# Performance work log

Hardware: AMD Instinct MI355X
Metric: run time of the kernel (lower is better)

The kernel has to match this reference:

```python
import jax, jax.numpy as jnp
import numpy as np

B, S, E, H = 2, 2048, 1024, 16
D = E // H  # head_dim = 64
NEG = -1e10


def setup_inputs() -> dict:
    key = jax.random.key(0)
    ks = jax.random.split(key, 12)
    sc = 1.0 / np.sqrt(E)
    return {
        "query": jax.random.normal(ks[0], (B, S, E), jnp.float32),
        "key_": jax.random.normal(ks[1], (B, S, E), jnp.float32),
        "value": jax.random.normal(ks[2], (B, S, E), jnp.float32),
        "mask": jax.random.randint(ks[3], (B, S), 0, 2, jnp.int32),
        "Wq": jax.random.normal(ks[4], (E, E), jnp.float32) * sc,
        "bq": jnp.zeros((E,), jnp.float32),
        "Wk": jax.random.normal(ks[5], (E, E), jnp.float32) * sc,
        "bk": jnp.zeros((E,), jnp.float32),
        "Wv": jax.random.normal(ks[6], (E, E), jnp.float32) * sc,
        "bv": jnp.zeros((E,), jnp.float32),
        "Wo": jax.random.normal(ks[7], (E, E), jnp.float32) * sc,
        "bo": jnp.zeros((E,), jnp.float32),
    }


def reference(query, key_, value, mask, Wq, bq, Wk, bk, Wv, bv, Wo, bo):
    # Linear projections (torch Linear: x @ W^T + b)
    Q = (query @ Wq.T + bq).reshape(B, S, H, D)
    K = (key_ @ Wk.T + bk).reshape(B, S, H, D)
    V = (value @ Wv.T + bv).reshape(B, S, H, D)
    # [B, H, Sq, Sk] scores
    scores = jnp.einsum("bqhd,bkhd->bhqk", Q, K) / jnp.sqrt(jnp.float32(D))
    # Original sets rows of masked query positions AND columns of masked key
    # positions to -1e10 (set, not add; overlapping assignment is same value).
    pad = (mask == 0)  # [B, S]
    bad = pad[:, :, None] | pad[:, None, :]  # [B, Sq, Sk]
    scores = scores + jnp.where(bad, NEG, 0.0)[:, None, :, :]
    weights = jax.nn.softmax(scores, axis=-1)
    out = jnp.einsum("bhqk,bkhd->bqhd", weights, V).reshape(B, S, E)
    return out @ Wo.T + bo
```

## Files before the change

kernel.cpp:

```cpp
#include <hip/hip_runtime.h>

typedef __attribute__((ext_vector_type(4)))  float          f32x4;
typedef __attribute__((ext_vector_type(16))) float          f32x16;
typedef __attribute__((ext_vector_type(8)))  short          s16x8;
typedef __attribute__((ext_vector_type(4)))  unsigned short u16x4;
typedef __attribute__((ext_vector_type(8)))  unsigned short u16x8;

#define MFMA_BF16(a, b, c) __builtin_amdgcn_mfma_f32_16x16x32_bf16((a), (b), (c), 0, 0, 0)
#define MFMA32(a, b, c)    __builtin_amdgcn_mfma_f32_32x32x16_bf16((a), (b), (c), 0, 0, 0)

static constexpr int Bb = 2, Ss = 2048, Ee = 1024, Hh = 16, Dd = 64;
static constexpr size_t M4 = 4u * 1024 * 1024;
static constexpr size_t M1 = 1024 * 1024;

__device__ __forceinline__ unsigned short f2b(float f) {
    unsigned u = __builtin_bit_cast(unsigned, f);
    u += 0x7fffu + ((u >> 16) & 1u);
    return (unsigned short)(u >> 16);
}

__device__ __forceinline__ void gld_lds16(const unsigned short* g, unsigned short* l) {
    __builtin_amdgcn_global_load_lds(
        (const __attribute__((address_space(1))) unsigned int*)g,
        (__attribute__((address_space(3))) unsigned int*)l, 16, 0, 0);
}

struct CvtArgs { const float* src[7]; unsigned short* dst; };

__global__ __launch_bounds__(256) void cvt_bf16(CvtArgs a)
{
    size_t i = ((size_t)blockIdx.x * 256 + threadIdx.x) * 8;
    int seg; size_t off;
    if (i < 3 * M4) { seg = (int)(i / M4);          off = i % M4; }
    else            { size_t j = i - 3 * M4;
                      seg = 3 + (int)(j / M1);      off = j % M1; }
    const float* s = a.src[seg] + off;
    f32x4 x0 = *(const f32x4*)s;
    f32x4 x1 = *(const f32x4*)(s + 4);
    u16x8 o = (u16x8){f2b(x0[0]), f2b(x0[1]), f2b(x0[2]), f2b(x0[3]),
                      f2b(x1[0]), f2b(x1[1]), f2b(x1[2]), f2b(x1[3])};
    *(u16x8*)(a.dst + i) = o;
}

template <int OUT_MODE>
__device__ __forceinline__ void gemm_bf16_body(const unsigned short* __restrict__ A,
                                               const unsigned short* __restrict__ W,
                                               const float* __restrict__ bias,
                                               void* __restrict__ Cv)
{
    __shared__ __align__(16) unsigned short Al[128 * 32];
    __shared__ __align__(16) unsigned short Bl[128 * 32];

    const int tid  = threadIdx.x;
    const int lane = tid & 63;
    const int wid  = tid >> 6;
    const int quad = lane >> 4;
    const int lr   = lane & 15;
    const int wr   = (wid >> 1) * 64;
    const int wc   = (wid & 1) * 64;
    const int m0   = blockIdx.y * 128;
    const int n0   = blockIdx.x * 128;

    const int srow = wid * 32 + (lane >> 2);
    const int sk8  = (lane & 3) * 8;
    const unsigned short* gA = A + (size_t)(m0 + srow) * 1024 + sk8;
    const unsigned short* gW = W + (size_t)(n0 + srow) * 1024 + sk8;
    unsigned short* lA = &Al[wid * 1024];
    unsigned short* lW = &Bl[wid * 1024];

    f32x4 acc[4][4];
#pragma unroll
    for (int i = 0; i < 4; i++)
#pragma unroll
        for (int j = 0; j < 4; j++) acc[i][j] = (f32x4){0.f, 0.f, 0.f, 0.f};

    for (int ks = 0; ks < 1024; ks += 32) {
        __syncthreads();
        gld_lds16(gA + ks,              lA);
        gld_lds16(gA + ks + 16 * 1024,  lA + 512);
        gld_lds16(gW + ks,              lW);
        gld_lds16(gW + ks + 16 * 1024,  lW + 512);
        __syncthreads();

        s16x8 af[4], bf[4];
#pragma unroll
        for (int t = 0; t < 4; t++) {
            af[t] = *(const s16x8*)&Al[(wr + t * 16 + lr) * 32 + quad * 8];
            bf[t] = *(const s16x8*)&Bl[(wc + t * 16 + lr) * 32 + quad * 8];
        }
#pragma unroll
        for (int mt = 0; mt < 4; mt++)
#pragma unroll
            for (int nt = 0; nt < 4; nt++)
                acc[mt][nt] = MFMA_BF16(af[mt], bf[nt], acc[mt][nt]);
    }

#pragma unroll
    for (int mt = 0; mt < 4; mt++)
#pragma unroll
        for (int nt = 0; nt < 4; nt++) {
            int   col  = n0 + wc + nt * 16 + lr;
            float bcol = bias[col];
            int   rbase = m0 + wr + mt * 16 + quad * 4;
            if (OUT_MODE == 2) {
                int bb = rbase >> 11, s = rbase & 2047;
                u16x4 pk;
#pragma unroll
                for (int r = 0; r < 4; r++) pk[r] = f2b(acc[mt][nt][r] + bcol);
                *(u16x4*)&((unsigned short*)Cv)[((size_t)(bb * 1024 + col)) * 2048 + s] = pk;
            } else {
#pragma unroll
                for (int r = 0; r < 4; r++) {
                    float v = acc[mt][nt][r] + bcol;
                    if (OUT_MODE == 3) v *= 0.125f;
                    if (OUT_MODE == 0)
                        ((float*)Cv)[(size_t)(rbase + r) * 1024 + col] = v;
                    else
                        ((unsigned short*)Cv)[(size_t)(rbase + r) * 1024 + col] = f2b(v);
                }
            }
        }
}

struct GArgs {
    const unsigned short* A[3];
    const unsigned short* W[3];
    const float* bias[3];
    unsigned short* C[3];
};

__global__ __launch_bounds__(256) void proj_gemm(GArgs ga)
{
    int z = blockIdx.z;
    if (z == 2)
        gemm_bf16_body<2>(ga.A[2], ga.W[2], ga.bias[2], ga.C[2]);
    else if (z == 1)
        gemm_bf16_body<1>(ga.A[1], ga.W[1], ga.bias[1], ga.C[1]);
    else
        gemm_bf16_body<3>(ga.A[0], ga.W[0], ga.bias[0], ga.C[0]);
}

__global__ __launch_bounds__(256) void out_gemm(const unsigned short* __restrict__ A,
                                                const unsigned short* __restrict__ W,
                                                const float* __restrict__ bias,
                                                float* __restrict__ C)
{
    gemm_bf16_body<0>(A, W, bias, C);
}

__global__ __launch_bounds__(256)
void flash_attn(const unsigned short* __restrict__ Q,
                const unsigned short* __restrict__ K,
                const unsigned short* __restrict__ Vt,
                const int* __restrict__ mask,
                unsigned short* __restrict__ O)
{
    constexpr int   ST  = 72;
    constexpr float EPS = 9.31322575e-10f;
    __shared__ __align__(16) unsigned short Kl[64 * ST];
    __shared__ __align__(16) unsigned short Vl[64 * ST];
    __shared__ __align__(16) unsigned short Pl[128 * ST];
    __shared__ __align__(16) float mkf[2048];
    __shared__ float lsq[128];

    const int b  = blockIdx.z;
    const int h  = blockIdx.y;
    const int q0 = blockIdx.x * 128;

    const int tid  = threadIdx.x;
    const int lane = tid & 63;
    const int wid  = tid >> 6;
    const int l31  = lane & 31;
    const int hl   = lane >> 5;

    for (int i = tid; i < 2048; i += 256) mkf[i] = mask[b * 2048 + i] ? 1.f : 0.f;

    const unsigned short* qg =
        Q + (size_t)(b * 2048 + q0 + wid * 32 + l31) * 1024 + h * 64 + hl * 8;
    s16x8 qf[4];
#pragma unroll
    for (int db = 0; db < 4; db++) qf[db] = *(const s16x8*)(qg + db * 16);

    __syncthreads();
    const float mq = mkf[q0 + wid * 32 + l31];

    const int lk = (tid >> 3) * ST + (tid & 7) * 8;
    const unsigned short* gK = K  + (size_t)(b * 2048 + (tid >> 3)) * 1024 + h * 64 + (tid & 7) * 8;
    const unsigned short* gV = Vt + (size_t)(b * 1024 + h * 64 + (tid >> 3)) * 2048 + (tid & 7) * 8;

    float  lsum  = 0.f;
    f32x16 accO0 = (f32x16){0.f,0.f,0.f,0.f,0.f,0.f,0.f,0.f,0.f,0.f,0.f,0.f,0.f,0.f,0.f,0.f};
    f32x16 accO1 = accO0;

    unsigned short* plw = &Pl[wid * 32 * ST];

    for (int kt = 0; kt < 2048; kt += 64) {
        __syncthreads();
        *(u16x8*)&Kl[lk]           = *(const u16x8*)(gK + (size_t)kt * 1024);
        *(u16x8*)&Kl[lk + 32 * ST] = *(const u16x8*)(gK + (size_t)(kt + 32) * 1024);
        *(u16x8*)&Vl[lk]           = *(const u16x8*)(gV + kt);
        *(u16x8*)&Vl[lk + 32 * ST] = *(const u16x8*)(gV + kt + (size_t)32 * 2048);
        __syncthreads();

#pragma unroll
        for (int kt2 = 0; kt2 < 2; kt2++) {
            f32x16 st = (f32x16){0.f,0.f,0.f,0.f,0.f,0.f,0.f,0.f,
                                 0.f,0.f,0.f,0.f,0.f,0.f,0.f,0.f};
#pragma unroll
            for (int db = 0; db < 4; db++) {
                s16x8 kf = *(const s16x8*)&Kl[(kt2 * 32 + l31) * ST + db * 16 + hl * 8];
                st = MFMA32(kf, qf[db], st);
            }
#pragma unroll
            for (int rq = 0; rq < 4; rq++) {
                int   kb = kt2 * 32 + 4 * hl + 8 * rq;
                f32x4 m4 = *(const f32x4*)&mkf[kt + kb];
                unsigned u[4];
#pragma unroll
                for (int r = 0; r < 4; r++) {
                    float e = __expf(st[rq * 4 + r]);
                    float p = e * (m4[r] * mq) + EPS;
                    lsum += p;
                    u[r] = __builtin_bit_cast(unsigned, p) + 0x8000u;
                }
                uint2 w;
                w.x = __builtin_amdgcn_perm(u[1], u[0], 0x07060302u);
                w.y = __builtin_amdgcn_perm(u[3], u[2], 0x07060302u);
                *(uint2*)&plw[l31 * ST + kb] = w;
            }
        }

#pragma unroll
        for (int kb = 0; kb < 4; kb++) {
            s16x8 pf  = *(const s16x8*)&plw[l31 * ST + kb * 16 + hl * 8];
            s16x8 vf0 = *(const s16x8*)&Vl[l31 * ST + kb * 16 + hl * 8];
            s16x8 vf1 = *(const s16x8*)&Vl[(32 + l31) * ST + kb * 16 + hl * 8];
            accO0 = MFMA32(pf, vf0, accO0);
            accO1 = MFMA32(pf, vf1, accO1);
        }
    }

    lsum += __shfl_xor(lsum, 32, 64);
    if (lane < 32) lsq[wid * 32 + l31] = lsum;

#pragma unroll
    for (int dc = 0; dc < 2; dc++)
#pragma unroll
        for (int rq = 0; rq < 4; rq++) {
            f32x4 ls4 = *(const f32x4*)&lsq[wid * 32 + 4 * hl + 8 * rq];
#pragma unroll
            for (int r = 0; r < 4; r++) {
                int   qrow = 4 * hl + 8 * rq + r;
                float acc  = (dc == 0) ? accO0[rq * 4 + r] : accO1[rq * 4 + r];
                float val  = acc * __builtin_amdgcn_rcpf(ls4[r]);
                O[(size_t)(b * 2048 + q0 + wid * 32 + qrow) * 1024 + h * 64 +
                  dc * 32 + l31] = f2b(val);
            }
        }
}

extern "C" void kernel_launch(void* const* d_in, const int* in_sizes, int n_in,
                              void* d_out, int out_size, void* d_ws, size_t ws_size,
                              hipStream_t stream)
{
    const float* query = (const float*)d_in[0];
    const float* key_  = (const float*)d_in[1];
    const float* value = (const float*)d_in[2];
    const int*   mask  = (const int*)d_in[3];
    const float* Wq    = (const float*)d_in[4];
    const float* bq    = (const float*)d_in[5];
    const float* Wk    = (const float*)d_in[6];
    const float* bk    = (const float*)d_in[7];
    const float* Wv    = (const float*)d_in[8];
    const float* bv    = (const float*)d_in[9];
    const float* Wo    = (const float*)d_in[10];
    const float* bo    = (const float*)d_in[11];
    float* out = (float*)d_out;

    unsigned short* cvt = (unsigned short*)d_ws;
    unsigned short* Aq  = cvt;
    unsigned short* Ak  = cvt + M4;
    unsigned short* Av  = cvt + 2 * M4;
    unsigned short* Wqb = cvt + 3 * M4;
    unsigned short* Wkb = Wqb + M1;
    unsigned short* Wvb = Wkb + M1;
    unsigned short* Wob = Wvb + M1;
    unsigned short* Qb  = Wob + M1;
    unsigned short* Kb  = Qb + M4;
    unsigned short* Vt  = Kb + M4;
    unsigned short* Ab  = Vt + M4;

    CvtArgs ca;
    ca.src[0] = query; ca.src[1] = key_; ca.src[2] = value;
    ca.src[3] = Wq; ca.src[4] = Wk; ca.src[5] = Wv; ca.src[6] = Wo;
    ca.dst = cvt;
    cvt_bf16<<<dim3(8192), 256, 0, stream>>>(ca);

    GArgs ga;
    ga.A[0] = Aq;  ga.A[1] = Ak;  ga.A[2] = Av;
    ga.W[0] = Wqb; ga.W[1] = Wkb; ga.W[2] = Wvb;
    ga.bias[0] = bq; ga.bias[1] = bk; ga.bias[2] = bv;
    ga.C[0] = Qb; ga.C[1] = Kb; ga.C[2] = Vt;
    proj_gemm<<<dim3(8, 32, 3), 256, 0, stream>>>(ga);

    flash_attn<<<dim3(Ss / 128, Hh, Bb), 256, 0, stream>>>(Qb, Kb, Vt, mask, Ab);
    out_gemm<<<dim3(8, 32, 1), 256, 0, stream>>>(Ab, Wob, bo, out);
}
```

Baseline: 272.8 us.

## Halve attention query tile, precompute float mask, widen GEMM K-step, use exp2

After: 272.6 us. Within noise of the previous version (-0.1%).

```diff
diff --git a/kernel.cpp b/kernel.cpp
--- a/kernel.cpp
+++ b/kernel.cpp
@@ -25,15 +25,24 @@
         (__attribute__((address_space(3))) unsigned int*)l, 16, 0, 0);
 }
 
-struct CvtArgs { const float* src[7]; unsigned short* dst; };
+struct CvtArgs { const float* src[7]; unsigned short* dst;
+                 const int* mask; float* maskf; };
 
 __global__ __launch_bounds__(256) void cvt_bf16(CvtArgs a)
 {
+    if (blockIdx.x == 8192) {
+#pragma unroll
+        for (int j = 0; j < 16; j++) {
+            int idx = threadIdx.x + j * 256;
+            a.maskf[idx] = a.mask[idx] ? 1.f : 0.f;
+        }
+        return;
+    }
     size_t i = ((size_t)blockIdx.x * 256 + threadIdx.x) * 8;
     int seg; size_t off;
-    if (i < 3 * M4) { seg = (int)(i / M4);          off = i % M4; }
+    if (i < 3 * M4) { seg = (int)(i / M4);     off = i % M4; }
     else            { size_t j = i - 3 * M4;
-                      seg = 3 + (int)(j / M1);      off = j % M1; }
+                      seg = 3 + (int)(j / M1); off = j % M1; }
     const float* s = a.src[seg] + off;
     f32x4 x0 = *(const f32x4*)s;
     f32x4 x1 = *(const f32x4*)(s + 4);
@@ -48,8 +57,8 @@
                                                const float* __restrict__ bias,
                                                void* __restrict__ Cv)
 {
-    __shared__ __align__(16) unsigned short Al[128 * 32];
-    __shared__ __align__(16) unsigned short Bl[128 * 32];
+    __shared__ __align__(16) unsigned short Al0[128 * 32], Al1[128 * 32];
+    __shared__ __align__(16) unsigned short Bl0[128 * 32], Bl1[128 * 32];
 
     const int tid  = threadIdx.x;
     const int lane = tid & 63;
@@ -65,8 +74,8 @@
     const int sk8  = (lane & 3) * 8;
     const unsigned short* gA = A + (size_t)(m0 + srow) * 1024 + sk8;
     const unsigned short* gW = W + (size_t)(n0 + srow) * 1024 + sk8;
-    unsigned short* lA = &Al[wid * 1024];
-    unsigned short* lW = &Bl[wid * 1024];
+    unsigned short* lA0 = &Al0[wid * 1024]; unsigned short* lA1 = &Al1[wid * 1024];
+    unsigned short* lW0 = &Bl0[wid * 1024]; unsigned short* lW1 = &Bl1[wid * 1024];
 
     f32x4 acc[4][4];
 #pragma unroll
@@ -74,25 +83,34 @@
 #pragma unroll
         for (int j = 0; j < 4; j++) acc[i][j] = (f32x4){0.f, 0.f, 0.f, 0.f};
 
-    for (int ks = 0; ks < 1024; ks += 32) {
-        __syncthreads();
-        gld_lds16(gA + ks,              lA);
-        gld_lds16(gA + ks + 16 * 1024,  lA + 512);
-        gld_lds16(gW + ks,              lW);
-        gld_lds16(gW + ks + 16 * 1024,  lW + 512);
-        __syncthreads();
-
-        s16x8 af[4], bf[4];
-#pragma unroll
-        for (int t = 0; t < 4; t++) {
-            af[t] = *(const s16x8*)&Al[(wr + t * 16 + lr) * 32 + quad * 8];
-            bf[t] = *(const s16x8*)&Bl[(wc + t * 16 + lr) * 32 + quad * 8];
-        }
-#pragma unroll
-        for (int mt = 0; mt < 4; mt++)
-#pragma unroll
-            for (int nt = 0; nt < 4; nt++)
-                acc[mt][nt] = MFMA_BF16(af[mt], bf[nt], acc[mt][nt]);
+    for (int ks = 0; ks < 1024; ks += 64) {
+        __syncthreads();
+        gld_lds16(gA + ks,                   lA0);
+        gld_lds16(gA + ks + 16 * 1024,       lA0 + 512);
+        gld_lds16(gA + ks + 32,              lA1);
+        gld_lds16(gA + ks + 32 + 16 * 1024,  lA1 + 512);
+        gld_lds16(gW + ks,                   lW0);
+        gld_lds16(gW + ks + 16 * 1024,       lW0 + 512);
+        gld_lds16(gW + ks + 32,              lW1);
+        gld_lds16(gW + ks + 32 + 16 * 1024,  lW1 + 512);
+        __syncthreads();
+
+#pragma unroll
+        for (int sub = 0; sub < 2; sub++) {
+            const unsigned short* Als = sub ? Al1 : Al0;
+            const unsigned short* Bls = sub ? Bl1 : Bl0;
+            s16x8 af[4], bf[4];
+#pragma unroll
+            for (int t = 0; t < 4; t++) {
+                af[t] = *(const s16x8*)&Als[(wr + t * 16 + lr) * 32 + quad * 8];
+                bf[t] = *(const s16x8*)&Bls[(wc + t * 16 + lr) * 32 + quad * 8];
+            }
+#pragma unroll
+            for (int mt = 0; mt < 4; mt++)
+#pragma unroll
+                for (int nt = 0; nt < 4; nt++)
+                    acc[mt][nt] = MFMA_BF16(af[mt], bf[nt], acc[mt][nt]);
+        }
     }
 
 #pragma unroll
@@ -112,7 +130,7 @@
 #pragma unroll
                 for (int r = 0; r < 4; r++) {
                     float v = acc[mt][nt][r] + bcol;
-                    if (OUT_MODE == 3) v *= 0.125f;
+                    if (OUT_MODE == 3) v *= 0.180336884f;
                     if (OUT_MODE == 0)
                         ((float*)Cv)[(size_t)(rbase + r) * 1024 + col] = v;
                     else
@@ -132,12 +150,9 @@
 __global__ __launch_bounds__(256) void proj_gemm(GArgs ga)
 {
     int z = blockIdx.z;
-    if (z == 2)
-        gemm_bf16_body<2>(ga.A[2], ga.W[2], ga.bias[2], ga.C[2]);
-    else if (z == 1)
-        gemm_bf16_body<1>(ga.A[1], ga.W[1], ga.bias[1], ga.C[1]);
-    else
-        gemm_bf16_body<3>(ga.A[0], ga.W[0], ga.bias[0], ga.C[0]);
+    if (z == 2)      gemm_bf16_body<2>(ga.A[2], ga.W[2], ga.bias[2], ga.C[2]);
+    else if (z == 1) gemm_bf16_body<1>(ga.A[1], ga.W[1], ga.bias[1], ga.C[1]);
+    else             gemm_bf16_body<3>(ga.A[0], ga.W[0], ga.bias[0], ga.C[0]);
 }
 
 __global__ __launch_bounds__(256) void out_gemm(const unsigned short* __restrict__ A,
@@ -152,47 +167,44 @@
 void flash_attn(const unsigned short* __restrict__ Q,
                 const unsigned short* __restrict__ K,
                 const unsigned short* __restrict__ Vt,
-                const int* __restrict__ mask,
+                const float* __restrict__ maskf,
                 unsigned short* __restrict__ O)
 {
-    constexpr int   ST  = 72;
+    constexpr int   ST  = 76;
     constexpr float EPS = 9.31322575e-10f;
     __shared__ __align__(16) unsigned short Kl[64 * ST];
     __shared__ __align__(16) unsigned short Vl[64 * ST];
-    __shared__ __align__(16) unsigned short Pl[128 * ST];
-    __shared__ __align__(16) float mkf[2048];
-    __shared__ float lsq[128];
+    __shared__ __align__(16) unsigned short Pl[64 * ST];
+    __shared__ float lsq[4][32];
 
     const int b  = blockIdx.z;
     const int h  = blockIdx.y;
-    const int q0 = blockIdx.x * 128;
+    const int q0 = blockIdx.x * 64;
 
     const int tid  = threadIdx.x;
     const int lane = tid & 63;
     const int wid  = tid >> 6;
     const int l31  = lane & 31;
     const int hl   = lane >> 5;
-
-    for (int i = tid; i < 2048; i += 256) mkf[i] = mask[b * 2048 + i] ? 1.f : 0.f;
+    const int qh   = wid & 1;
+    const int kh   = wid >> 1;
 
     const unsigned short* qg =
-        Q + (size_t)(b * 2048 + q0 + wid * 32 + l31) * 1024 + h * 64 + hl * 8;
+        Q + (size_t)(b * 2048 + q0 + qh * 32 + l31) * 1024 + h * 64 + hl * 8;
     s16x8 qf[4];
 #pragma unroll
     for (int db = 0; db < 4; db++) qf[db] = *(const s16x8*)(qg + db * 16);
 
-    __syncthreads();
-    const float mq = mkf[q0 + wid * 32 + l31];
+    const float  mq  = maskf[b * 2048 + q0 + qh * 32 + l31];
+    const float* mkp = maskf + b * 2048;
 
     const int lk = (tid >> 3) * ST + (tid & 7) * 8;
     const unsigned short* gK = K  + (size_t)(b * 2048 + (tid >> 3)) * 1024 + h * 64 + (tid & 7) * 8;
     const unsigned short* gV = Vt + (size_t)(b * 1024 + h * 64 + (tid >> 3)) * 2048 + (tid & 7) * 8;
 
-    float  lsum  = 0.f;
-    f32x16 accO0 = (f32x16){0.f,0.f,0.f,0.f,0.f,0.f,0.f,0.f,0.f,0.f,0.f,0.f,0.f,0.f,0.f,0.f};
-    f32x16 accO1 = accO0;
-
-    unsigned short* plw = &Pl[wid * 32 * ST];
+    float  lsum = 0.f;
+    f32x16 accO = (f32x16){0.f,0.f,0.f,0.f,0.f,0.f,0.f,0.f,
+                           0.f,0.f,0.f,0.f,0.f,0.f,0.f,0.f};
 
     for (int kt = 0; kt < 2048; kt += 64) {
         __syncthreads();
@@ -202,61 +214,56 @@
         *(u16x8*)&Vl[lk + 32 * ST] = *(const u16x8*)(gV + kt + (size_t)32 * 2048);
         __syncthreads();
 
-#pragma unroll
-        for (int kt2 = 0; kt2 < 2; kt2++) {
-            f32x16 st = (f32x16){0.f,0.f,0.f,0.f,0.f,0.f,0.f,0.f,
-                                 0.f,0.f,0.f,0.f,0.f,0.f,0.f,0.f};
-#pragma unroll
-            for (int db = 0; db < 4; db++) {
-                s16x8 kf = *(const s16x8*)&Kl[(kt2 * 32 + l31) * ST + db * 16 + hl * 8];
-                st = MFMA32(kf, qf[db], st);
+        f32x16 st = (f32x16){0.f,0.f,0.f,0.f,0.f,0.f,0.f,0.f,
+                             0.f,0.f,0.f,0.f,0.f,0.f,0.f,0.f};
+#pragma unroll
+        for (int db = 0; db < 4; db++) {
+            s16x8 kf = *(const s16x8*)&Kl[(kh * 32 + l31) * ST + db * 16 + hl * 8];
+            st = MFMA32(kf, qf[db], st);
+        }
+#pragma unroll
+        for (int rq = 0; rq < 4; rq++) {
+            int   kb = 4 * hl + 8 * rq;
+            f32x4 m4 = *(const f32x4*)&mkp[kt + kh * 32 + kb];
+            unsigned u[4];
+#pragma unroll
+            for (int r = 0; r < 4; r++) {
+                float e = __builtin_amdgcn_exp2f(st[rq * 4 + r]);
+                float p = e * (m4[r] * mq) + EPS;
+                lsum += p;
+                u[r] = __builtin_bit_cast(unsigned, p) + 0x8000u;
             }
-#pragma unroll
-            for (int rq = 0; rq < 4; rq++) {
-                int   kb = kt2 * 32 + 4 * hl + 8 * rq;
-                f32x4 m4 = *(const f32x4*)&mkf[kt + kb];
-                unsigned u[4];
-#pragma unroll
-                for (int r = 0; r < 4; r++) {
-                    float e = __expf(st[rq * 4 + r]);
-                    float p = e * (m4[r] * mq) + EPS;
-                    lsum += p;
-                    u[r] = __builtin_bit_cast(unsigned, p) + 0x8000u;
-                }
-                uint2 w;
-                w.x = __builtin_amdgcn_perm(u[1], u[0], 0x07060302u);
-                w.y = __builtin_amdgcn_perm(u[3], u[2], 0x07060302u);
-                *(uint2*)&plw[l31 * ST + kb] = w;
-            }
-        }
-
-#pragma unroll
-        for (int kb = 0; kb < 4; kb++) {
-            s16x8 pf  = *(const s16x8*)&plw[l31 * ST + kb * 16 + hl * 8];
-            s16x8 vf0 = *(const s16x8*)&Vl[l31 * ST + kb * 16 + hl * 8];
-            s16x8 vf1 = *(const s16x8*)&Vl[(32 + l31) * ST + kb * 16 + hl * 8];
-            accO0 = MFMA32(pf, vf0, accO0);
-            accO1 = MFMA32(pf, vf1, accO1);
+            uint2 w;
+            w.x = __builtin_amdgcn_perm(u[1], u[0], 0x07060302u);
+            w.y = __builtin_amdgcn_perm(u[3], u[2], 0x07060302u);
+            *(uint2*)&Pl[(qh * 32 + l31) * ST + kh * 32 + kb] = w;
+        }
+        __syncthreads();
+
+#pragma unroll
+        for (int ks = 0; ks < 4; ks++) {
+            s16x8 pf = *(const s16x8*)&Pl[(qh * 32 + l31) * ST + ks * 16 + hl * 8];
+            s16x8 vf = *(const s16x8*)&Vl[(kh * 32 + l31) * ST + ks * 16 + hl * 8];
+            accO = MFMA32(pf, vf, accO);
         }
     }
 
     lsum += __shfl_xor(lsum, 32, 64);
-    if (lane < 32) lsq[wid * 32 + l31] = lsum;
-
-#pragma unroll
-    for (int dc = 0; dc < 2; dc++)
-#pragma unroll
-        for (int rq = 0; rq < 4; rq++) {
-            f32x4 ls4 = *(const f32x4*)&lsq[wid * 32 + 4 * hl + 8 * rq];
-#pragma unroll
-            for (int r = 0; r < 4; r++) {
-                int   qrow = 4 * hl + 8 * rq + r;
-                float acc  = (dc == 0) ? accO0[rq * 4 + r] : accO1[rq * 4 + r];
-                float val  = acc * __builtin_amdgcn_rcpf(ls4[r]);
-                O[(size_t)(b * 2048 + q0 + wid * 32 + qrow) * 1024 + h * 64 +
-                  dc * 32 + l31] = f2b(val);
-            }
-        }
+    lsq[wid][l31] = lsum;
+    __syncthreads();
+
+#pragma unroll
+    for (int rq = 0; rq < 4; rq++) {
+        int   qr = 4 * hl + 8 * rq;
+        f32x4 lA = *(const f32x4*)&lsq[qh][qr];
+        f32x4 lB = *(const f32x4*)&lsq[qh + 2][qr];
+#pragma unroll
+        for (int r = 0; r < 4; r++) {
+            float val = accO[rq * 4 + r] * __builtin_amdgcn_rcpf(lA[r] + lB[r]);
+            O[(size_t)(b * 2048 + q0 + qh * 32 + qr + r) * 1024 + h * 64 +
+              kh * 32 + l31] = f2b(val);
+        }
+    }
 }
 
 extern "C" void kernel_launch(void* const* d_in, const int* in_sizes, int n_in,
@@ -289,12 +296,13 @@
     unsigned short* Kb  = Qb + M4;
     unsigned short* Vt  = Kb + M4;
     unsigned short* Ab  = Vt + M4;
+    float*          mkf = (float*)(Ab + M4);
 
     CvtArgs ca;
     ca.src[0] = query; ca.src[1] = key_; ca.src[2] = value;
     ca.src[3] = Wq; ca.src[4] = Wk; ca.src[5] = Wv; ca.src[6] = Wo;
-    ca.dst = cvt;
-    cvt_bf16<<<dim3(8192), 256, 0, stream>>>(ca);
+    ca.dst = cvt; ca.mask = mask; ca.maskf = mkf;
+    cvt_bf16<<<dim3(8193), 256, 0, stream>>>(ca);
 
     GArgs ga;
     ga.A[0] = Aq;  ga.A[1] = Ak;  ga.A[2] = Av;
@@ -303,6 +311,6 @@
     ga.C[0] = Qb; ga.C[1] = Kb; ga.C[2] = Vt;
     proj_gemm<<<dim3(8, 32, 3), 256, 0, stream>>>(ga);
 
-    flash_attn<<<dim3(Ss / 128, Hh, Bb), 256, 0, stream>>>(Qb, Kb, Vt, mask, Ab);
+    flash_attn<<<dim3(Ss / 64, Hh, Bb), 256, 0, stream>>>(Qb, Kb, Vt, mkf, Ab);
     out_gemm<<<dim3(8, 32, 1), 256, 0, stream>>>(Ab, Wob, bo, out);
 }
```
